# Performance work log

Measured on AMD Instinct MI355X. Metric: run time of the kernel, lower is better.

## Reference

```python
import jax, jax.numpy as jnp
import numpy as np

B, S, D, H = 2, 2048, 1024, 16
HD = D // H  # head_dim = 64


def setup_inputs() -> dict:
    key = jax.random.key(0)
    ks = jax.random.split(key, 12)
    xav = (2.0 / (D + D)) ** 0.5  # xavier_normal std for square Linear
    q = jax.random.normal(ks[0], (B, S, D), jnp.float32)
    k = jax.random.normal(ks[1], (B, S, D), jnp.float32)
    v = jax.random.normal(ks[2], (B, S, D), jnp.float32)
    Wq = jax.random.normal(ks[3], (D, D), jnp.float32) * xav
    Wk = jax.random.normal(ks[4], (D, D), jnp.float32) * xav
    Wv = jax.random.normal(ks[5], (D, D), jnp.float32) * xav
    bq = jnp.zeros((D,), jnp.float32)
    bk = jnp.zeros((D,), jnp.float32)
    bv = jnp.zeros((D,), jnp.float32)
    # valid-prefix padding masks (True = valid token); key 0 always valid so
    # no causal softmax row is fully masked (avoids NaN, matches real usage).
    klen = jax.random.randint(ks[6], (B,), S // 2, S + 1)
    qlen = jax.random.randint(ks[7], (B,), S // 2, S + 1)
    pos = jnp.arange(S)
    key_padding_mask = pos[None, :] < klen[:, None]
    query_padding_mask = pos[None, :] < qlen[:, None]
    return {
        "q": q, "k": k, "v": v,
        "Wq": Wq, "bq": bq, "Wk": Wk, "bk": bk, "Wv": Wv, "bv": bv,
        "key_padding_mask": key_padding_mask,
        "query_padding_mask": query_padding_mask,
    }


def _proj_split(x, W, b, n_heads):
    # Linear (y = x W^T + b) then split heads: [B,S,D] -> [B,H,S,hd]
    bsz, sq, dm = x.shape
    hd = dm // n_heads
    y = x @ W.T + b
    return y.reshape(bsz, sq, n_heads, hd).transpose(0, 2, 1, 3)


def reference(q, k, v, Wq, bq, Wk, bk, Wv, bv, key_padding_mask, query_padding_mask):
    bsz, sq, dm = q.shape
    sk = k.shape[1]
    Q = _proj_split(q, Wq, bq, H)  # [B,H,Sq,hd]
    K = _proj_split(k, Wk, bk, H)  # [B,H,Sk,hd]
    V = _proj_split(v, Wv, bv, H)  # [B,H,Sk,hd]
    scale = 1.0 / jnp.sqrt(jnp.asarray(Q.shape[-1], Q.dtype))
    scores = jnp.einsum('bhqd,bhkd->bhqk', Q, K) * scale  # [B,H,Sq,Sk]
    # key padding: -inf where key invalid
    scores = jnp.where(key_padding_mask[:, None, None, :], scores, -jnp.inf)
    # causal: -inf strictly above the diagonal
    causal_ok = jnp.tril(jnp.ones((sq, sk), bool))
    scores = jnp.where(causal_ok[None, None, :, :], scores, -jnp.inf)
    attn = jax.nn.softmax(scores, axis=-1)
    # q_mask: zero out rows for padded queries (post-softmax, as in source)
    attn = jnp.where(query_padding_mask[:, None, :, None], attn, 0.0)
    # dropout p=0.0 -> identity
    out = jnp.einsum('bhqk,bhkd->bhqd', attn, V)
    out = out.transpose(0, 2, 1, 3).reshape(bsz, sq, dm)
    return out + q
```

## Files before the change

kernel.cpp:

```cpp
#include <hip/hip_runtime.h>
#include <stdint.h>

#define BATCH 2
#define SEQ 2048
#define DMODEL 1024
#define NHEAD 16
#define HDIM 64
#define CVT_BLOCKS 15360

typedef __attribute__((ext_vector_type(8))) short bf16x8;
typedef __attribute__((ext_vector_type(4))) float f32x4;

__device__ __forceinline__ unsigned short f2bf(float f) {
  unsigned int u = __float_as_uint(f);
  u += 0x7fffu + ((u >> 16) & 1u);
  return (unsigned short)(u >> 16);
}
__device__ __forceinline__ unsigned int pk2bf(float a, float b) {
  return __builtin_amdgcn_perm(__float_as_uint(b) + 0x8000u,
                               __float_as_uint(a) + 0x8000u, 0x07060302u);
}
__device__ __forceinline__ void async_copy16(const void* g, void* l) {
  __builtin_amdgcn_global_load_lds(
      (const __attribute__((address_space(1))) void*)g,
      (__attribute__((address_space(3))) void*)l, 16, 0, 0);
}

__global__ __launch_bounds__(256) void cvt_all(
    const float* __restrict__ q, const float* __restrict__ k,
    const float* __restrict__ v, const float* __restrict__ Wq,
    const float* __restrict__ Wk, const float* __restrict__ Wv,
    unsigned short* __restrict__ dst,
    const unsigned char* __restrict__ kp, const unsigned char* __restrict__ qp,
    int* __restrict__ lens) {
  if (blockIdx.x == CVT_BLOCKS) {
    const int t = threadIdx.x, wave = t >> 6, lane = t & 63;
    const unsigned char* base = (wave < 2) ? kp : qp;
    const int b = wave & 1;
    const bool bytefmt = (base[1] != 0);
    int cnt = 0;
    if (bytefmt) {
      const uint4* p = (const uint4*)(base + (size_t)b * SEQ);
#pragma unroll
      for (int g = 0; g < 2; g++) {
        const uint4 x = p[g * 64 + lane];
        const unsigned int w[4] = {x.x, x.y, x.z, x.w};
#pragma unroll
        for (int i = 0; i < 4; i++) {
          const unsigned int ww = w[i];
          cnt += ((ww & 0xffu) != 0) + ((ww & 0xff00u) != 0) +
                 ((ww & 0xff0000u) != 0) + ((ww & 0xff000000u) != 0);
        }
      }
    } else {
      const uint4* p = (const uint4*)(base + (size_t)b * SEQ * 4);
#pragma unroll
      for (int g = 0; g < 8; g++) {
        const uint4 x = p[g * 64 + lane];
        cnt += (x.x != 0) + (x.y != 0) + (x.z != 0) + (x.w != 0);
      }
    }
#pragma unroll
    for (int off = 32; off >= 1; off >>= 1) cnt += __shfl_xor(cnt, off, 64);
    if (lane == 0) lens[wave] = cnt;
    return;
  }
  const int g = blockIdx.x * 256 + threadIdx.x;
  const float* src;
  size_t off, dbase;
  if (g < 3 * (1 << 20)) {
    const int ti = g >> 20;
    src = (ti == 0) ? q : (ti == 1) ? k : v;
    off = (size_t)(g & ((1 << 20) - 1));
    dbase = (size_t)ti << 22;
  } else {
    const int gw = g - 3 * (1 << 20);
    const int ti = gw >> 18;
    src = (ti == 0) ? Wq : (ti == 1) ? Wk : Wv;
    off = (size_t)(gw & ((1 << 18) - 1));
    dbase = (3ull << 22) + ((size_t)ti << 20);
  }
  const float4 x = ((const float4*)src)[off];
  ushort4 o;
  o.x = f2bf(x.x); o.y = f2bf(x.y); o.z = f2bf(x.z); o.w = f2bf(x.w);
  *(ushort4*)(dst + dbase + off * 4) = o;
}

__global__ __launch_bounds__(256) void qkv_proj(
    const unsigned short* __restrict__ xq, const unsigned short* __restrict__ xk,
    const unsigned short* __restrict__ xv,
    const unsigned short* __restrict__ Wq, const float* __restrict__ bq,
    const unsigned short* __restrict__ Wk, const float* __restrict__ bk,
    const unsigned short* __restrict__ Wv, const float* __restrict__ bv,
    unsigned short* __restrict__ Qo, unsigned short* __restrict__ Ko,
    unsigned short* __restrict__ Vo, const int* __restrict__ lens) {
  const int z = blockIdx.z;
  const int m0 = blockIdx.y * 128, n0 = blockIdx.x * 128;
  const int b = m0 >> 11;
  const int len = (z == 0) ? lens[2 + b] : lens[b];
  if ((m0 & (SEQ - 1)) >= len) return;

  const unsigned short* x = (z == 0) ? xq : (z == 1) ? xk : xv;
  const unsigned short* W = (z == 0) ? Wq : (z == 1) ? Wk : Wv;
  const float* bias = (z == 0) ? bq : (z == 1) ? bk : bv;
  unsigned short* dst = (z == 0) ? Qo : (z == 1) ? Ko : Vo;
  const float osc = (z == 0) ? 0.18033688011112042f : 1.0f;

  __shared__ unsigned short As[128 * 64];
  __shared__ unsigned short Bs[128 * 64];

  const int t = threadIdx.x;
  const int wave = t >> 6, lane = t & 63, quad = lane >> 4, l16 = lane & 15;
  const int wm = wave >> 1, wn = wave & 1;

  const f32x4 fz = {0.f, 0.f, 0.f, 0.f};
  f32x4 acc[4][4];
#pragma unroll
  for (int i = 0; i < 4; i++)
#pragma unroll
    for (int j = 0; j < 4; j++) acc[i][j] = fz;

  for (int k0 = 0; k0 < DMODEL; k0 += 64) {
    __syncthreads();
#pragma unroll
    for (int c = 0; c < 4; c++) {
      const int slot = c * 256 + t;
      const int row = slot >> 3, pg = slot & 7;
      const int lg = (pg ^ (row & 7)) * 8;
      async_copy16(x + (size_t)(m0 + row) * DMODEL + k0 + lg,
                   (char*)As + (c * 256 + (t & 192)) * 16);
      async_copy16(W + (size_t)(n0 + row) * DMODEL + k0 + lg,
                   (char*)Bs + (c * 256 + (t & 192)) * 16);
    }
    __syncthreads();
#pragma unroll
    for (int kk = 0; kk < 2; kk++) {
      bf16x8 af[4], bfr[4];
#pragma unroll
      for (int i = 0; i < 4; i++) {
        const int ra = wm * 64 + i * 16 + l16;
        const int rb = wn * 64 + i * 16 + l16;
        af[i] = *(const bf16x8*)(As + ra * 64 + ((kk * 4 + quad) ^ (ra & 7)) * 8);
        bfr[i] = *(const bf16x8*)(Bs + rb * 64 + ((kk * 4 + quad) ^ (rb & 7)) * 8);
      }
      if (z == 2) {
#pragma unroll
        for (int i = 0; i < 4; i++)
#pragma unroll
          for (int j = 0; j < 4; j++)
            acc[i][j] = __builtin_amdgcn_mfma_f32_16x16x32_bf16(af[i], bfr[j], acc[i][j], 0, 0, 0);
      } else {
#pragma unroll
        for (int i = 0; i < 4; i++)
#pragma unroll
          for (int j = 0; j < 4; j++)
            acc[i][j] = __builtin_amdgcn_mfma_f32_16x16x32_bf16(bfr[j], af[i], acc[i][j], 0, 0, 0);
      }
    }
  }

  if (z == 2) {
#pragma unroll
    for (int j = 0; j < 4; j++) {
      const int n = n0 + wn * 64 + j * 16 + l16;
      const float bb_ = bias[n];
      const int h = n >> 6, hd = n & 63;
#pragma unroll
      for (int i = 0; i < 4; i++) {
        const int s0 = (m0 & (SEQ - 1)) + wm * 64 + i * 16 + quad * 4;
        uint2 w;
        w.x = pk2bf(acc[i][j][0] + bb_, acc[i][j][1] + bb_);
        w.y = pk2bf(acc[i][j][2] + bb_, acc[i][j][3] + bb_);
        *(uint2*)(dst + (((size_t)(b * NHEAD + h) * HDIM + hd) << 11) + s0) = w;
      }
    }
  } else {
#pragma unroll
    for (int j = 0; j < 4; j++) {
      const int nb = n0 + wn * 64 + j * 16 + quad * 4;
      const float4 b4 = *(const float4*)(bias + nb);
      const int h = nb >> 6, hd0 = nb & 63;
#pragma unroll
      for (int i = 0; i < 4; i++) {
        const int s = (m0 & (SEQ - 1)) + wm * 64 + i * 16 + l16;
        uint2 w;
        w.x = pk2bf((acc[i][j][0] + b4.x) * osc, (acc[i][j][1] + b4.y) * osc);
        w.y = pk2bf((acc[i][j][2] + b4.z) * osc, (acc[i][j][3] + b4.w) * osc);
        *(uint2*)(dst + (((size_t)(b * NHEAD + h) * SEQ + s) << 6) + hd0) = w;
      }
    }
  }
}


template <bool MASKED>
__device__ __forceinline__ void softmax_update(
    const f32x4 s[8], int key0, int qrow, int klen, int quad, int l16,
    float& mst, float& lsum, f32x4 o[4], unsigned short* Pdst) {
  float pm[8][4];
  float rm = -__builtin_inff();
  if (MASKED) {
    const int kmax = ((qrow < klen - 1) ? qrow : klen - 1) - key0 - quad * 4;
#pragma unroll
    for (int nf = 0; nf < 8; nf++)
#pragma unroll
      for (int r = 0; r < 4; r++) {
        pm[nf][r] = (nf * 16 + r <= kmax) ? s[nf][r] : -__builtin_inff();
        rm = fmaxf(rm, pm[nf][r]);
      }
  } else {
#pragma unroll
    for (int nf = 0; nf < 8; nf++)
#pragma unroll
      for (int r = 0; r < 4; r++) {
        pm[nf][r] = s[nf][r];
        rm = fmaxf(rm, pm[nf][r]);
      }
  }
  rm = fmaxf(rm, __shfl_xor(rm, 16, 64));
  rm = fmaxf(rm, __shfl_xor(rm, 32, 64));
  if (__ballot(rm > mst) != 0ull) {
    const float mnew = fmaxf(mst, rm);
    const float alpha = exp2f(fmaxf(mst, -1e30f) - fmaxf(mnew, -1e30f));
    mst = mnew;
    lsum *= alpha;
    float ab[4];
#pragma unroll
    for (int r = 0; r < 4; r++) ab[r] = __shfl(alpha, quad * 4 + r, 64);
#pragma unroll
    for (int db = 0; db < 4; db++)
#pragma unroll
      for (int r = 0; r < 4; r++) o[db][r] *= ab[r];
  }
  const float mref = fmaxf(mst, -1e30f);
  float rs = 0.f;
#pragma unroll
  for (int nf = 0; nf < 8; nf++)
#pragma unroll
    for (int r = 0; r < 4; r++) {
      const float p = exp2f(pm[nf][r] - mref);
      pm[nf][r] = p;
      rs += p;
    }
  rs += __shfl_xor(rs, 16, 64);
  rs += __shfl_xor(rs, 32, 64);
  lsum += rs;
#pragma unroll
  for (int nf = 0; nf < 8; nf++) {
    uint2 w;
    w.x = pk2bf(pm[nf][0], pm[nf][1]);
    w.y = pk2bf(pm[nf][2], pm[nf][3]);
    const int grp = (nf * 2 + (quad >> 1)) ^ l16;
    *(uint2*)(Pdst + l16 * 128 + grp * 8 + (quad & 1) * 4) = w;
  }
}

template <bool MASKED>
__device__ __forceinline__ void tile_pass(
    const unsigned short* __restrict__ ks, const unsigned short* __restrict__ vt,
    unsigned short* __restrict__ Pw, bf16x8 qf0, bf16x8 qf1,
    int key0, int qrow, int klen, int quad, int l16,
    float& mst, float& lsum, f32x4 o[4]) {
  const f32x4 fz = {0.f, 0.f, 0.f, 0.f};
  f32x4 s[8];
#pragma unroll
  for (int nf = 0; nf < 8; nf++) {
    const int row = nf * 16 + l16;
    const int sw = row & 7;
    const bf16x8 kf0 = *(const bf16x8*)(ks + row * 64 + (quad ^ sw) * 8);
    const bf16x8 kf1 = *(const bf16x8*)(ks + row * 64 + ((quad + 4) ^ sw) * 8);
    f32x4 a = fz;
    a = __builtin_amdgcn_mfma_f32_16x16x32_bf16(kf0, qf0, a, 0, 0, 0);
    a = __builtin_amdgcn_mfma_f32_16x16x32_bf16(kf1, qf1, a, 0, 0, 0);
    s[nf] = a;
  }
  softmax_update<MASKED>(s, key0, qrow, klen, quad, l16, mst, lsum, o, Pw);
  bf16x8 pf[4];
#pragma unroll
  for (int ksn = 0; ksn < 4; ksn++)
    pf[ksn] = *(const bf16x8*)(Pw + l16 * 128 + ((ksn * 4 + quad) ^ l16) * 8);
#pragma unroll
  for (int db = 0; db < 4; db++) {
    const int d = db * 16 + l16;
#pragma unroll
    for (int ksn = 0; ksn < 4; ksn++) {
      const bf16x8 v = *(const bf16x8*)(vt + d * 128 + ((ksn * 4 + quad) ^ l16) * 8);
      o[db] = __builtin_amdgcn_mfma_f32_16x16x32_bf16(pf[ksn], v, o[db], 0, 0, 0);
    }
  }
}

__global__ __launch_bounds__(256, 3) void attn_kernel(
    const unsigned short* __restrict__ Qb, const unsigned short* __restrict__ Kb,
    const unsigned short* __restrict__ VTb, const float* __restrict__ qin,
    const int* __restrict__ lens, float* __restrict__ out) {
  const int pi = blockIdx.x, h = blockIdx.y, b = blockIdx.z;
  const int lo = pi, hi = 31 - pi;
  const int bh = b * NHEAD + h;
  const int t = threadIdx.x, wave = t >> 6, lane = t & 63, quad = lane >> 4, l16 = lane & 15;
  const int klen = lens[b], qlen = lens[2 + b];
  const bool doHI = (hi * 64 < qlen);

  __shared__ unsigned short Ks[128 * 64];
  __shared__ unsigned short VT[64 * 128];
  __shared__ unsigned short Ps[4][16 * 128];

  const unsigned short* Qp = Qb + (size_t)bh * SEQ * HDIM;
  const unsigned short* Kp = Kb + (size_t)bh * SEQ * HDIM;
  const unsigned short* Vt = VTb + (size_t)bh * HDIM * SEQ;

  const int qrLO = lo * 64 + wave * 16 + l16;
  const int qrHI = hi * 64 + wave * 16 + l16;
  const bf16x8 qlo0 = *(const bf16x8*)(Qp + (size_t)qrLO * HDIM + quad * 8);
  const bf16x8 qlo1 = *(const bf16x8*)(Qp + (size_t)qrLO * HDIM + 32 + quad * 8);
  const bf16x8 qhi0 = *(const bf16x8*)(Qp + (size_t)qrHI * HDIM + quad * 8);
  const bf16x8 qhi1 = *(const bf16x8*)(Qp + (size_t)qrHI * HDIM + 32 + quad * 8);

  const f32x4 fz = {0.f, 0.f, 0.f, 0.f};
  f32x4 oLO[4], oHI[4];
#pragma unroll
  for (int i = 0; i < 4; i++) { oLO[i] = fz; oHI[i] = fz; }
  float mLO = -__builtin_inff(), lLO = 0.f;
  float mHI = -__builtin_inff(), lHI = 0.f;

  const int kendLO = ((lo * 64 + 64) < klen) ? (lo * 64 + 64) : klen;
  const int ktotLO = (kendLO + 127) >> 7;
  int ktotHI = 0;
  if (doHI) {
    const int kendHI = ((hi * 64 + 64) < klen) ? (hi * 64 + 64) : klen;
    ktotHI = (kendHI + 127) >> 7;
  }
  const int ktot = (ktotHI > ktotLO) ? ktotHI : ktotLO;

  for (int kt = 0; kt < ktot; kt++) {
    const int key0 = kt << 7;
    __syncthreads();
#pragma unroll
    for (int c = 0; c < 4; c++) {
      const int slot = c * 256 + t;
      const int row = slot >> 3, pg = slot & 7;
      async_copy16(Kp + (size_t)(key0 + row) * HDIM + (pg ^ (row & 7)) * 8,
                   (char*)Ks + (c * 256 + (t & 192)) * 16);
    }
#pragma unroll
    for (int c = 0; c < 4; c++) {
      const int slot = c * 256 + t;
      const int row = slot >> 4, pg = slot & 15;
      async_copy16(Vt + (size_t)row * SEQ + key0 + (pg ^ (row & 15)) * 8,
                   (char*)VT + (c * 256 + (t & 192)) * 16);
    }
    __syncthreads();

    if (kt < ktotHI) {
      if ((key0 + 127 <= hi * 64) && (key0 + 127 < klen))
        tile_pass<false>(Ks, VT, Ps[wave], qhi0, qhi1, key0, qrHI, klen, quad, l16, mHI, lHI, oHI);
      else
        tile_pass<true>(Ks, VT, Ps[wave], qhi0, qhi1, key0, qrHI, klen, quad, l16, mHI, lHI, oHI);
    }
    if (kt < ktotLO) {
      if ((key0 + 127 <= lo * 64) && (key0 + 127 < klen))
        tile_pass<false>(Ks, VT, Ps[wave], qlo0, qlo1, key0, qrLO, klen, quad, l16, mLO, lLO, oLO);
      else
        tile_pass<true>(Ks, VT, Ps[wave], qlo0, qlo1, key0, qrLO, klen, quad, l16, mLO, lLO, oLO);
    }
  }

  const float invLO = (lLO > 0.f) ? 1.f / lLO : 0.f;
  const float invHI = (lHI > 0.f) ? 1.f / lHI : 0.f;
  float ibLO[4], ibHI[4];
#pragma unroll
  for (int r = 0; r < 4; r++) {
    ibLO[r] = __shfl(invLO, quad * 4 + r, 64);
    ibHI[r] = __shfl(invHI, quad * 4 + r, 64);
  }
#pragma unroll
  for (int db = 0; db < 4; db++) {
    const int col = h * HDIM + db * 16 + l16;
#pragma unroll
    for (int r = 0; r < 4; r++) {
      const int iL = lo * 64 + wave * 16 + quad * 4 + r;
      const int iH = hi * 64 + wave * 16 + quad * 4 + r;
      const size_t oL = (size_t)(b * SEQ + iL) * DMODEL + col;
      const size_t oH = (size_t)(b * SEQ + iH) * DMODEL + col;
      out[oL] = ((iL < qlen) ? oLO[db][r] * ibLO[r] : 0.f) + qin[oL];
      out[oH] = ((iH < qlen) ? oHI[db][r] * ibHI[r] : 0.f) + qin[oH];
    }
  }
}

extern "C" void kernel_launch(void* const* d_in, const int* in_sizes, int n_in,
                              void* d_out, int out_size, void* d_ws, size_t ws_size,
                              hipStream_t stream) {
  (void)in_sizes; (void)n_in; (void)out_size; (void)ws_size;
  const float* q = (const float*)d_in[0];
  const float* k = (const float*)d_in[1];
  const float* v = (const float*)d_in[2];
  const float* Wq = (const float*)d_in[3];
  const float* bq = (const float*)d_in[4];
  const float* Wk = (const float*)d_in[5];
  const float* bk = (const float*)d_in[6];
  const float* Wv = (const float*)d_in[7];
  const float* bv = (const float*)d_in[8];
  const unsigned char* kpm = (const unsigned char*)d_in[9];
  const unsigned char* qpm = (const unsigned char*)d_in[10];
  float* out = (float*)d_out;

  const size_t tsz = (size_t)BATCH * SEQ * DMODEL;
  const size_t wsz = (size_t)DMODEL * DMODEL;

  char* ws = (char*)d_ws;
  int* lens = (int*)ws;
  unsigned short* cvt_base = (unsigned short*)(ws + 256);
  unsigned short* qb16 = cvt_base;
  unsigned short* kb16 = qb16 + tsz;
  unsigned short* vb16 = kb16 + tsz;
  unsigned short* Wqb = vb16 + tsz;
  unsigned short* Wkb = Wqb + wsz;
  unsigned short* Wvb = Wkb + wsz;
  unsigned short* Qw = Wvb + wsz;
  unsigned short* Kw = Qw + tsz;
  unsigned short* Vtw = Kw + tsz;

  cvt_all<<<dim3(CVT_BLOCKS + 1), dim3(256), 0, stream>>>(q, k, v, Wq, Wk, Wv,
                                                          cvt_base, kpm, qpm, lens);
  qkv_proj<<<dim3(8, 32, 3), dim3(256), 0, stream>>>(qb16, kb16, vb16, Wqb, bq, Wkb, bk, Wvb, bv, Qw, Kw, Vtw, lens);
  attn_kernel<<<dim3(16, NHEAD, BATCH), dim3(256), 0, stream>>>(Qw, Kw, Vtw, q, lens, out);
}
```

Baseline: 210.2 us.

## Fuse fp32-to-bf16 conversion into QKV projection GEMM tile loads

Removes the separate conversion kernel that wrote bf16 copies of activations and weights, and instead loads fp32 directly in the projection GEMM, packing to bf16 in registers before storing to LDS. Mask length counting moves to a tiny standalone kernel. This eliminates a full read/write pass over inputs and weights, but doubles GEMM global load bytes and replaces asynchronous global-to-LDS copies with synchronous register loads. Rounding changes to round-half-up packing.

```diff
diff --git a/kernel.cpp b/kernel.cpp
--- a/kernel.cpp
+++ b/kernel.cpp
@@ -6,16 +6,10 @@
 #define DMODEL 1024
 #define NHEAD 16
 #define HDIM 64
-#define CVT_BLOCKS 15360
 
 typedef __attribute__((ext_vector_type(8))) short bf16x8;
 typedef __attribute__((ext_vector_type(4))) float f32x4;
 
-__device__ __forceinline__ unsigned short f2bf(float f) {
-  unsigned int u = __float_as_uint(f);
-  u += 0x7fffu + ((u >> 16) & 1u);
-  return (unsigned short)(u >> 16);
-}
 __device__ __forceinline__ unsigned int pk2bf(float a, float b) {
   return __builtin_amdgcn_perm(__float_as_uint(b) + 0x8000u,
                                __float_as_uint(a) + 0x8000u, 0x07060302u);
@@ -26,72 +20,46 @@
       (__attribute__((address_space(3))) void*)l, 16, 0, 0);
 }
 
-__global__ __launch_bounds__(256) void cvt_all(
-    const float* __restrict__ q, const float* __restrict__ k,
-    const float* __restrict__ v, const float* __restrict__ Wq,
-    const float* __restrict__ Wk, const float* __restrict__ Wv,
-    unsigned short* __restrict__ dst,
+__global__ __launch_bounds__(256) void lens_kernel(
     const unsigned char* __restrict__ kp, const unsigned char* __restrict__ qp,
     int* __restrict__ lens) {
-  if (blockIdx.x == CVT_BLOCKS) {
-    const int t = threadIdx.x, wave = t >> 6, lane = t & 63;
-    const unsigned char* base = (wave < 2) ? kp : qp;
-    const int b = wave & 1;
-    const bool bytefmt = (base[1] != 0);
-    int cnt = 0;
-    if (bytefmt) {
-      const uint4* p = (const uint4*)(base + (size_t)b * SEQ);
-#pragma unroll
-      for (int g = 0; g < 2; g++) {
-        const uint4 x = p[g * 64 + lane];
-        const unsigned int w[4] = {x.x, x.y, x.z, x.w};
-#pragma unroll
-        for (int i = 0; i < 4; i++) {
-          const unsigned int ww = w[i];
-          cnt += ((ww & 0xffu) != 0) + ((ww & 0xff00u) != 0) +
-                 ((ww & 0xff0000u) != 0) + ((ww & 0xff000000u) != 0);
-        }
-      }
-    } else {
-      const uint4* p = (const uint4*)(base + (size_t)b * SEQ * 4);
-#pragma unroll
-      for (int g = 0; g < 8; g++) {
-        const uint4 x = p[g * 64 + lane];
-        cnt += (x.x != 0) + (x.y != 0) + (x.z != 0) + (x.w != 0);
-      }
-    }
-#pragma unroll
-    for (int off = 32; off >= 1; off >>= 1) cnt += __shfl_xor(cnt, off, 64);
-    if (lane == 0) lens[wave] = cnt;
-    return;
-  }
-  const int g = blockIdx.x * 256 + threadIdx.x;
-  const float* src;
-  size_t off, dbase;
-  if (g < 3 * (1 << 20)) {
-    const int ti = g >> 20;
-    src = (ti == 0) ? q : (ti == 1) ? k : v;
-    off = (size_t)(g & ((1 << 20) - 1));
-    dbase = (size_t)ti << 22;
+  const int t = threadIdx.x, wave = t >> 6, lane = t & 63;
+  const unsigned char* base = (wave < 2) ? kp : qp;
+  const int b = wave & 1;
+  const bool bytefmt = (base[1] != 0);
+  int cnt = 0;
+  if (bytefmt) {
+    const uint4* p = (const uint4*)(base + (size_t)b * SEQ);
+#pragma unroll
+    for (int g = 0; g < 2; g++) {
+      const uint4 x = p[g * 64 + lane];
+      const unsigned int w[4] = {x.x, x.y, x.z, x.w};
+#pragma unroll
+      for (int i = 0; i < 4; i++) {
+        const unsigned int ww = w[i];
+        cnt += ((ww & 0xffu) != 0) + ((ww & 0xff00u) != 0) +
+               ((ww & 0xff0000u) != 0) + ((ww & 0xff000000u) != 0);
+      }
+    }
   } else {
-    const int gw = g - 3 * (1 << 20);
-    const int ti = gw >> 18;
-    src = (ti == 0) ? Wq : (ti == 1) ? Wk : Wv;
-    off = (size_t)(gw & ((1 << 18) - 1));
-    dbase = (3ull << 22) + ((size_t)ti << 20);
-  }
-  const float4 x = ((const float4*)src)[off];
-  ushort4 o;
-  o.x = f2bf(x.x); o.y = f2bf(x.y); o.z = f2bf(x.z); o.w = f2bf(x.w);
-  *(ushort4*)(dst + dbase + off * 4) = o;
+    const uint4* p = (const uint4*)(base + (size_t)b * SEQ * 4);
+#pragma unroll
+    for (int g = 0; g < 8; g++) {
+      const uint4 x = p[g * 64 + lane];
+      cnt += (x.x != 0) + (x.y != 0) + (x.z != 0) + (x.w != 0);
+    }
+  }
+#pragma unroll
+  for (int off = 32; off >= 1; off >>= 1) cnt += __shfl_xor(cnt, off, 64);
+  if (lane == 0) lens[wave] = cnt;
 }
 
 __global__ __launch_bounds__(256) void qkv_proj(
-    const unsigned short* __restrict__ xq, const unsigned short* __restrict__ xk,
-    const unsigned short* __restrict__ xv,
-    const unsigned short* __restrict__ Wq, const float* __restrict__ bq,
-    const unsigned short* __restrict__ Wk, const float* __restrict__ bk,
-    const unsigned short* __restrict__ Wv, const float* __restrict__ bv,
+    const float* __restrict__ xq, const float* __restrict__ xk,
+    const float* __restrict__ xv,
+    const float* __restrict__ Wq, const float* __restrict__ bq,
+    const float* __restrict__ Wk, const float* __restrict__ bk,
+    const float* __restrict__ Wv, const float* __restrict__ bv,
     unsigned short* __restrict__ Qo, unsigned short* __restrict__ Ko,
     unsigned short* __restrict__ Vo, const int* __restrict__ lens) {
   const int z = blockIdx.z;
@@ -100,8 +68,8 @@
   const int len = (z == 0) ? lens[2 + b] : lens[b];
   if ((m0 & (SEQ - 1)) >= len) return;
 
-  const unsigned short* x = (z == 0) ? xq : (z == 1) ? xk : xv;
-  const unsigned short* W = (z == 0) ? Wq : (z == 1) ? Wk : Wv;
+  const float* x = (z == 0) ? xq : (z == 1) ? xk : xv;
+  const float* W = (z == 0) ? Wq : (z == 1) ? Wk : Wv;
   const float* bias = (z == 0) ? bq : (z == 1) ? bk : bv;
   unsigned short* dst = (z == 0) ? Qo : (z == 1) ? Ko : Vo;
   const float osc = (z == 0) ? 0.18033688011112042f : 1.0f;
@@ -127,10 +95,19 @@
       const int slot = c * 256 + t;
       const int row = slot >> 3, pg = slot & 7;
       const int lg = (pg ^ (row & 7)) * 8;
-      async_copy16(x + (size_t)(m0 + row) * DMODEL + k0 + lg,
-                   (char*)As + (c * 256 + (t & 192)) * 16);
-      async_copy16(W + (size_t)(n0 + row) * DMODEL + k0 + lg,
-                   (char*)Bs + (c * 256 + (t & 192)) * 16);
+      const float* xa = x + (size_t)(m0 + row) * DMODEL + k0 + lg;
+      const float* wb = W + (size_t)(n0 + row) * DMODEL + k0 + lg;
+      const float4 f0 = *(const float4*)xa;
+      const float4 f1 = *(const float4*)(xa + 4);
+      const float4 g0 = *(const float4*)wb;
+      const float4 g1 = *(const float4*)(wb + 4);
+      uint4 wa, wbv;
+      wa.x = pk2bf(f0.x, f0.y); wa.y = pk2bf(f0.z, f0.w);
+      wa.z = pk2bf(f1.x, f1.y); wa.w = pk2bf(f1.z, f1.w);
+      wbv.x = pk2bf(g0.x, g0.y); wbv.y = pk2bf(g0.z, g0.w);
+      wbv.z = pk2bf(g1.x, g1.y); wbv.w = pk2bf(g1.z, g1.w);
+      *(uint4*)((char*)As + slot * 16) = wa;
+      *(uint4*)((char*)Bs + slot * 16) = wbv;
     }
     __syncthreads();
 #pragma unroll
@@ -406,23 +383,14 @@
   float* out = (float*)d_out;
 
   const size_t tsz = (size_t)BATCH * SEQ * DMODEL;
-  const size_t wsz = (size_t)DMODEL * DMODEL;
 
   char* ws = (char*)d_ws;
   int* lens = (int*)ws;
-  unsigned short* cvt_base = (unsigned short*)(ws + 256);
-  unsigned short* qb16 = cvt_base;
-  unsigned short* kb16 = qb16 + tsz;
-  unsigned short* vb16 = kb16 + tsz;
-  unsigned short* Wqb = vb16 + tsz;
-  unsigned short* Wkb = Wqb + wsz;
-  unsigned short* Wvb = Wkb + wsz;
-  unsigned short* Qw = Wvb + wsz;
+  unsigned short* Qw = (unsigned short*)(ws + 256);
   unsigned short* Kw = Qw + tsz;
   unsigned short* Vtw = Kw + tsz;
 
-  cvt_all<<<dim3(CVT_BLOCKS + 1), dim3(256), 0, stream>>>(q, k, v, Wq, Wk, Wv,
-                                                          cvt_base, kpm, qpm, lens);
-  qkv_proj<<<dim3(8, 32, 3), dim3(256), 0, stream>>>(qb16, kb16, vb16, Wqb, bq, Wkb, bk, Wvb, bv, Qw, Kw, Vtw, lens);
+  lens_kernel<<<dim3(1), dim3(256), 0, stream>>>(kpm, qpm, lens);
+  qkv_proj<<<dim3(8, 32, 3), dim3(256), 0, stream>>>(q, k, v, Wq, bq, Wk, bk, Wv, bv, Qw, Kw, Vtw, lens);
   attn_kernel<<<dim3(16, NHEAD, BATCH), dim3(256), 0, stream>>>(Qw, Kw, Vtw, q, lens, out);
 }
```

Measured after the change: 231.6 us. 1.1x slower.
